# Optimization experiments

Hardware: AMD Instinct MI355X
Metric: run time of the kernel (lower is better)

## Reference

```python
import jax, jax.numpy as jnp
import numpy as np

E = 8          # num_experts
H = 1024       # hidden_size
F = 2048       # ffn_dim per expert
T = 8192       # total tokens (sorted by expert, T % E == 0)


def setup_inputs() -> dict:
    key = jax.random.key(0)
    k1, k2, k3, k4 = jax.random.split(key, 4)
    x = jax.random.normal(k1, (T, H), dtype=jnp.float32)
    # tokens are pre-sorted by expert with an equal split (dropless, balanced topo)
    expert_idx = (jnp.arange(T, dtype=jnp.int64) * E) // T
    w1 = jax.random.normal(k2, (E, F, H), dtype=jnp.float32) * 0.02
    v1 = jax.random.normal(k3, (E, F, H), dtype=jnp.float32) * 0.02
    w2 = jax.random.normal(k4, (E, F, H), dtype=jnp.float32) * 0.02
    return {"x": x, "expert_idx": expert_idx, "w1": w1, "v1": v1, "w2": w2}


def reference(x, expert_idx, w1, v1, w2):
    # Block-sparse SDD/DSD GLU with tokens grouped contiguously by expert
    # (expert_idx is sorted with equal counts), so the sparse matmuls reduce
    # to grouped batched GEMMs over the expert axis.
    tpe = x.shape[0] // w1.shape[0]          # tokens per expert
    xg = x.reshape(E, tpe, H)                # [E, tpe, H]
    # sdd(x, w1^T, topo): per-expert x @ w1_e^T  -> [E, tpe, F]
    h1 = jnp.einsum('eth,efh->etf', xg, w1)
    h2 = jnp.einsum('eth,efh->etf', xg, v1)
    # exact (erf) GELU to match torch.nn.functional.gelu default
    g = jax.nn.gelu(h1, approximate=False) * h2
    # dsd(x1, w2): per-expert g @ w2_e -> [E, tpe, H]
    out = jnp.einsum('etf,efh->eth', g, w2)
    return out.reshape(x.shape[0], H)
```

## Files before the change

kernel.cpp:

```cpp
#include <hip/hip_runtime.h>
#include <hip/hip_bf16.h>
#include <cstdint>
#include <cstddef>

#define NE 8
#define NH 1024
#define NF 2048
#define NT 8192
#define TPE (NT / NE)
#define NKT (NH / 64)
#define NKT2 (NF / 64)

typedef uint16_t u16;
typedef uint32_t u32;
typedef __attribute__((ext_vector_type(8))) __bf16 bf16x8;
typedef __attribute__((ext_vector_type(4))) float f32x4;

__device__ __forceinline__ u16 f2bf_rn(float f) {
  u32 u = __float_as_uint(f);
  u32 r = (u + 0x7fffu + ((u >> 16) & 1u)) >> 16;
  return (u16)r;
}

__global__ void cvt_f32_bf16(const float* __restrict__ in, u16* __restrict__ out, int n) {
  int i = (blockIdx.x * blockDim.x + threadIdx.x) * 4;
  if (i < n) {
    float4 v = *reinterpret_cast<const float4*>(in + i);
    ushort4 o;
    o.x = f2bf_rn(v.x);
    o.y = f2bf_rn(v.y);
    o.z = f2bf_rn(v.z);
    o.w = f2bf_rn(v.w);
    *reinterpret_cast<ushort4*>(out + i) = o;
  }
}

__global__ void pack_b(const float* __restrict__ w1, const float* __restrict__ v1,
                       u16* __restrict__ bc) {
  int j = blockIdx.x;
  int e = j >> 12;
  int r = j & 4095;
  int p = r >> 5;
  int q = (r >> 4) & 1;
  int c = r & 15;
  const float* src = (q ? v1 : w1) + ((size_t)e * NF + p * 16 + c) * NH;
  u16* dst = bc + (size_t)j * NH;
  int i = threadIdx.x * 4;
  float4 v = *reinterpret_cast<const float4*>(src + i);
  ushort4 o;
  o.x = f2bf_rn(v.x);
  o.y = f2bf_rn(v.y);
  o.z = f2bf_rn(v.z);
  o.w = f2bf_rn(v.w);
  *reinterpret_cast<ushort4*>(dst + i) = o;
}

__global__ void transpose_w2(const float* __restrict__ w2, u16* __restrict__ w2t) {
  __shared__ float tile[32][33];
  const int e = blockIdx.z;
  const int h0 = blockIdx.x * 32;
  const int f0 = blockIdx.y * 32;
  const int tx = threadIdx.x, ty = threadIdx.y;
  const float* src = w2 + ((size_t)e * NF + f0) * NH + h0;
#pragma unroll
  for (int i = 0; i < 4; i++) {
    int r = ty + i * 8;
    tile[r][tx] = src[(size_t)r * NH + tx];
  }
  __syncthreads();
  u16* dst = w2t + ((size_t)e * NH + h0) * NF + f0;
#pragma unroll
  for (int i = 0; i < 4; i++) {
    int r = ty + i * 8;
    dst[(size_t)r * NF + tx] = f2bf_rn(tile[tx][r]);
  }
}

__device__ __forceinline__ void async_lds16(const u16* g, const u16* lds) {
  __builtin_amdgcn_global_load_lds(
      (const __attribute__((address_space(1))) u32*)g,
      (__attribute__((address_space(3))) u32*)lds, 16, 0, 0);
}

__device__ __forceinline__ float one_plus_erf(float s) {
  float z = fabsf(s);
  float t = __builtin_amdgcn_rcpf(fmaf(0.3275911f, z, 1.0f));
  float p = t * fmaf(t, fmaf(t, fmaf(t, fmaf(t, 1.061405429f, -1.453152027f),
                                     1.421413741f), -0.284496736f), 0.254829592f);
  float pe = p * __expf(-z * z);
  return (s >= 0.0f) ? (2.0f - pe) : pe;
}

#define MFMA16(ACC, A, B)                                                      \
  _Pragma("unroll") for (int m = 0; m < 4; m++)                                \
    _Pragma("unroll") for (int n = 0; n < 2; n++) {                            \
      ACC[m][n] = __builtin_amdgcn_mfma_f32_16x16x32_bf16(A[m][0], B[n][0],    \
                                                          ACC[m][n], 0, 0, 0); \
      ACC[m][n] = __builtin_amdgcn_mfma_f32_16x16x32_bf16(A[m][1], B[n][1],    \
                                                          ACC[m][n], 0, 0, 0); \
    }

#define LD(OFF) (*reinterpret_cast<const bf16x8*>(Lb + (OFF)))

#define STAGE(GP, DST)                         \
  {                                            \
    async_lds16((GP) + g0, Lb + (DST) + s0);   \
    async_lds16((GP) + g1, Lb + (DST) + s1);   \
  }

__launch_bounds__(512, 2)
__global__ void glu_gemm8(const u16* __restrict__ xb, const u16* __restrict__ bc,
                          u16* __restrict__ gb) {
  __shared__ __align__(16) u16 L[2 * 2 * 2 * 8192];
  u16* Lb = &L[0];

  const int wg = blockIdx.x;
  const int sw = (wg & 7) * 64 + (wg >> 3);
  const int e = sw >> 6;
  const int by = (sw >> 4) & 3;
  const int bx = sw & 15;
  const int m0 = e * TPE + by * 256;
  const int n0 = bx * 256;

  const int tid = threadIdx.x;
  const int lane = tid & 63;
  const int wid = tid >> 6;
  const int qr = wid >> 2;
  const int qc = wid & 3;
  const int fr = lane & 15;
  const int kq = (lane >> 4) * 8;
  const int msk = (fr & 7) << 3;

  int aK0 = (qr * 64 + fr) * 64 + (kq ^ msk);
  int aK1 = (qr * 64 + fr) * 64 + ((32 + kq) ^ msk);
  int bK0 = 16384 + (qc * 32 + fr) * 64 + (kq ^ msk);
  int bK1 = 16384 + (qc * 32 + fr) * 64 + ((32 + kq) ^ msk);

  const int s0 = tid * 8;
  const int s1 = (512 + tid) * 8;
  const int r0 = s0 >> 6, r1 = s1 >> 6;
  const int g0 = r0 * NH + ((s0 & 63) ^ ((r0 & 7) << 3));
  const int g1 = r1 * NH + ((s1 & 63) ^ ((r1 & 7) << 3));

  const u16* Abase = xb + (size_t)m0 * NH;
  const u16* Bbase = bc + ((size_t)e * (2 * NF) + n0) * NH;

  f32x4 acc[2][2][4][2] = {};

  STAGE(Abase, 0);
  STAGE(Bbase, 16384);
  STAGE(Bbase + (size_t)128 * NH, 24576);
  STAGE(Abase + (size_t)128 * NH, 8192);
  STAGE(Abase + 64, 32768);
  STAGE(Bbase + (size_t)128 * NH + 64, 32768 + 24576);
  asm volatile("s_waitcnt vmcnt(4)" ::: "memory");
  __builtin_amdgcn_s_barrier();

  int bfo = 0;
#pragma unroll 1
  for (int t = 0; t < NKT; t++) {
    const int nbo = bfo ^ 32768;
    bf16x8 a_[4][2], b0_[2][2], b1_[2][2];

#pragma unroll
    for (int m = 0; m < 4; m++) {
      a_[m][0] = LD(aK0 + m * 1024);
      a_[m][1] = LD(aK1 + m * 1024);
    }
#pragma unroll
    for (int n = 0; n < 2; n++) {
      b0_[n][0] = LD(bK0 + n * 1024);
      b0_[n][1] = LD(bK1 + n * 1024);
    }
    if (t + 1 < NKT) STAGE(Abase + (size_t)128 * NH + (t + 1) * 64, nbo + 8192);
    __builtin_amdgcn_s_barrier();
    __builtin_amdgcn_s_setprio(1);
    MFMA16(acc[0][0], a_, b0_);
    __builtin_amdgcn_s_setprio(0);
    __builtin_amdgcn_s_barrier();

#pragma unroll
    for (int n = 0; n < 2; n++) {
      b1_[n][0] = LD(bK0 + 8192 + n * 1024);
      b1_[n][1] = LD(bK1 + 8192 + n * 1024);
    }
    if (t + 1 < NKT) STAGE(Bbase + (t + 1) * 64, nbo + 16384);
    __builtin_amdgcn_s_barrier();
    __builtin_amdgcn_s_setprio(1);
    MFMA16(acc[0][1], a_, b1_);
    __builtin_amdgcn_s_setprio(0);
    __builtin_amdgcn_s_barrier();

#pragma unroll
    for (int m = 0; m < 4; m++) {
      a_[m][0] = LD(aK0 + 8192 + m * 1024);
      a_[m][1] = LD(aK1 + 8192 + m * 1024);
    }
    if (t + 2 < NKT) STAGE(Abase + (t + 2) * 64, bfo);
    __builtin_amdgcn_s_barrier();
    __builtin_amdgcn_s_setprio(1);
    MFMA16(acc[1][1], a_, b1_);
    __builtin_amdgcn_s_setprio(0);
    __builtin_amdgcn_s_barrier();

    if (t + 2 < NKT) STAGE(Bbase + (size_t)128 * NH + (t + 2) * 64, bfo + 24576);
    __builtin_amdgcn_s_barrier();
    __builtin_amdgcn_s_setprio(1);
    MFMA16(acc[1][0], a_, b0_);
    __builtin_amdgcn_s_setprio(0);
    if (t + 2 < NKT)      asm volatile("s_waitcnt vmcnt(4)" ::: "memory");
    else if (t + 1 < NKT) asm volatile("s_waitcnt vmcnt(0)" ::: "memory");
    __builtin_amdgcn_s_barrier();
    aK0 ^= 32768; aK1 ^= 32768; bK0 ^= 32768; bK1 ^= 32768;
    bfo = nbo;
  }

  const int rq = (lane >> 4) * 4;
#pragma unroll
  for (int QR = 0; QR < 2; QR++)
#pragma unroll
    for (int QC = 0; QC < 2; QC++)
#pragma unroll
      for (int m = 0; m < 4; m++) {
        int row = m0 + QR * 128 + qr * 64 + m * 16 + rq;
        int f = ((n0 + QC * 128 + qc * 32) >> 1) + fr;
#pragma unroll
        for (int r = 0; r < 4; r++) {
          float h1 = acc[QR][QC][m][0][r];
          float h2 = acc[QR][QC][m][1][r];
          float g = 0.5f * h1 * one_plus_erf(h1 * 0.70710678118654752f) * h2;
          gb[(size_t)(row + r) * NF + f] = f2bf_rn(g);
        }
      }
}

__launch_bounds__(512, 2)
__global__ void down_gemm8(const u16* __restrict__ gb, const u16* __restrict__ w2tb,
                           float* __restrict__ out) {
  __shared__ __align__(16) u16 L[2 * 4 * 8192];
  u16* Lb = &L[0];

  const int wg = blockIdx.x;
  const int sw = (wg & 7) * 32 + (wg >> 3);
  const int e = sw >> 5;
  const int loc = sw & 31;
  const int bm = loc >> 2;
  const int bn = loc & 3;
  const int m0 = e * TPE + bm * 128;
  const int n0 = bn * 256;

  const int tid = threadIdx.x;
  const int lane = tid & 63;
  const int wid = tid >> 6;
  const int qr = wid >> 2;
  const int qc = wid & 3;
  const int fr = lane & 15;
  const int kq = (lane >> 4) * 8;
  const int msk = (fr & 7) << 3;

  int aK0 = (qr * 64 + fr) * 64 + (kq ^ msk);
  int aK1 = (qr * 64 + fr) * 64 + ((32 + kq) ^ msk);
  int bK0 = 8192 + (qc * 32 + fr) * 64 + (kq ^ msk);
  int bK1 = 8192 + (qc * 32 + fr) * 64 + ((32 + kq) ^ msk);

  const int s0 = tid * 8;
  const int s1 = (512 + tid) * 8;
  const int r0 = s0 >> 6, r1 = s1 >> 6;
  const int g0 = r0 * NF + ((s0 & 63) ^ ((r0 & 7) << 3));
  const int g1 = r1 * NF + ((s1 & 63) ^ ((r1 & 7) << 3));

  const u16* Ab = gb + (size_t)m0 * NF;
  const u16* Bb = w2tb + ((size_t)e * NH + n0) * NF;

  f32x4 acc[2][4][2] = {};

  STAGE(Ab, 0);
  STAGE(Bb, 8192);
  STAGE(Bb + (size_t)128 * NF, 16384);
  asm volatile("s_waitcnt vmcnt(2)" ::: "memory");
  __builtin_amdgcn_s_barrier();

  int bfo = 0;
#pragma unroll 1
  for (int t = 0; t < NKT2; t++) {
    const int nbo = bfo ^ 32768;
    bf16x8 a_[4][2], b_[2][2];

#pragma unroll
    for (int m = 0; m < 4; m++) {
      a_[m][0] = LD(aK0 + m * 1024);
      a_[m][1] = LD(aK1 + m * 1024);
    }
#pragma unroll
    for (int n = 0; n < 2; n++) {
      b_[n][0] = LD(bK0 + n * 1024);
      b_[n][1] = LD(bK1 + n * 1024);
    }
    if (t + 1 < NKT2) {
      STAGE(Ab + (t + 1) * 64, nbo);
      STAGE(Bb + (t + 1) * 64, nbo + 8192);
    }
    __builtin_amdgcn_s_barrier();
    __builtin_amdgcn_s_setprio(1);
    MFMA16(acc[0], a_, b_);
    __builtin_amdgcn_s_setprio(0);
    if (t + 1 < NKT2) asm volatile("s_waitcnt vmcnt(4)" ::: "memory");
    else              asm volatile("s_waitcnt vmcnt(0)" ::: "memory");
    __builtin_amdgcn_s_barrier();

#pragma unroll
    for (int n = 0; n < 2; n++) {
      b_[n][0] = LD(bK0 + 8192 + n * 1024);
      b_[n][1] = LD(bK1 + 8192 + n * 1024);
    }
    if (t + 1 < NKT2) STAGE(Bb + (size_t)128 * NF + (t + 1) * 64, nbo + 16384);
    __builtin_amdgcn_s_barrier();
    __builtin_amdgcn_s_setprio(1);
    MFMA16(acc[1], a_, b_);
    __builtin_amdgcn_s_setprio(0);
    if (t + 1 < NKT2) asm volatile("s_waitcnt vmcnt(2)" ::: "memory");
    __builtin_amdgcn_s_barrier();
    aK0 ^= 32768; aK1 ^= 32768; bK0 ^= 32768; bK1 ^= 32768;
    bfo = nbo;
  }

  const int rq = (lane >> 4) * 4;
#pragma unroll
  for (int QC = 0; QC < 2; QC++)
#pragma unroll
    for (int m = 0; m < 4; m++) {
      int row = m0 + qr * 64 + m * 16 + rq;
#pragma unroll
      for (int n = 0; n < 2; n++) {
        int col = n0 + QC * 128 + qc * 32 + n * 16 + fr;
#pragma unroll
        for (int r = 0; r < 4; r++)
          out[(size_t)(row + r) * NH + col] = acc[QC][m][n][r];
      }
    }
}

extern "C" void kernel_launch(void* const* d_in, const int* in_sizes, int n_in,
                              void* d_out, int out_size, void* d_ws, size_t ws_size,
                              hipStream_t stream) {
  const float* x = (const float*)d_in[0];
  const float* w1 = (const float*)d_in[2];
  const float* v1 = (const float*)d_in[3];
  const float* w2 = (const float*)d_in[4];
  float* out = (float*)d_out;

  char* ws = (char*)d_ws;
  u16* xb   = (u16*)(ws);
  u16* bc   = (u16*)(ws + (size_t)16 * 1024 * 1024);
  u16* w2tb = (u16*)(ws + (size_t)80 * 1024 * 1024);
  u16* gb   = (u16*)(ws + (size_t)112 * 1024 * 1024);

  const int nx = NT * NH;

  cvt_f32_bf16<<<nx / 4 / 256, 256, 0, stream>>>(x, xb, nx);
  pack_b<<<NE * 2 * NF, 256, 0, stream>>>(w1, v1, bc);
  transpose_w2<<<dim3(NH / 32, NF / 32, NE), dim3(32, 8, 1), 0, stream>>>(w2, w2tb);

  glu_gemm8<<<512, 512, 0, stream>>>(xb, bc, gb);
  down_gemm8<<<256, 512, 0, stream>>>(gb, w2tb, out);
}
```

Before: 175.2 us.

## Fuse prep kernels and make GLU GEMM persistent over two N tiles

Merges the three fp32-to-bf16 conversion/packing/transpose kernels into one launch with a block-index dispatch, removing two kernel launches. The GLU GEMM now runs 256 workgroups that each compute two 256-wide N tiles in sequence. The second tile's prologue loads are issued before the first tile's GELU epilogue and stores, so that global traffic overlaps the epilogue. This costs half the grid parallelism (256 blocks, one per CU) and adds register pressure from keeping the epilogue live while loads are in flight.

```diff
diff --git a/kernel.cpp b/kernel.cpp
--- a/kernel.cpp
+++ b/kernel.cpp
@@ -22,57 +22,57 @@
   return (u16)r;
 }
 
-__global__ void cvt_f32_bf16(const float* __restrict__ in, u16* __restrict__ out, int n) {
-  int i = (blockIdx.x * blockDim.x + threadIdx.x) * 4;
-  if (i < n) {
-    float4 v = *reinterpret_cast<const float4*>(in + i);
+#define PACK_NB 32768
+#define CVT_NB 8192
+#define TR_NB 16384
+
+__global__ void prep(const float* __restrict__ x, const float* __restrict__ w1,
+                     const float* __restrict__ v1, const float* __restrict__ w2,
+                     u16* __restrict__ xb, u16* __restrict__ bc, u16* __restrict__ w2t) {
+  __shared__ float tile[32][33];
+  const int bid = blockIdx.x;
+  const int tid = threadIdx.x;
+
+  if (bid < PACK_NB) {
+    int j = bid;
+    int e = j >> 12;
+    int r = j & 4095;
+    int p = r >> 5;
+    int q = (r >> 4) & 1;
+    int c = r & 15;
+    const float* src = (q ? v1 : w1) + ((size_t)e * NF + p * 16 + c) * NH;
+    u16* dst = bc + (size_t)j * NH;
+    int i = tid * 4;
+    float4 v = *reinterpret_cast<const float4*>(src + i);
     ushort4 o;
-    o.x = f2bf_rn(v.x);
-    o.y = f2bf_rn(v.y);
-    o.z = f2bf_rn(v.z);
-    o.w = f2bf_rn(v.w);
-    *reinterpret_cast<ushort4*>(out + i) = o;
-  }
-}
-
-__global__ void pack_b(const float* __restrict__ w1, const float* __restrict__ v1,
-                       u16* __restrict__ bc) {
-  int j = blockIdx.x;
-  int e = j >> 12;
-  int r = j & 4095;
-  int p = r >> 5;
-  int q = (r >> 4) & 1;
-  int c = r & 15;
-  const float* src = (q ? v1 : w1) + ((size_t)e * NF + p * 16 + c) * NH;
-  u16* dst = bc + (size_t)j * NH;
-  int i = threadIdx.x * 4;
-  float4 v = *reinterpret_cast<const float4*>(src + i);
-  ushort4 o;
-  o.x = f2bf_rn(v.x);
-  o.y = f2bf_rn(v.y);
-  o.z = f2bf_rn(v.z);
-  o.w = f2bf_rn(v.w);
-  *reinterpret_cast<ushort4*>(dst + i) = o;
-}
-
-__global__ void transpose_w2(const float* __restrict__ w2, u16* __restrict__ w2t) {
-  __shared__ float tile[32][33];
-  const int e = blockIdx.z;
-  const int h0 = blockIdx.x * 32;
-  const int f0 = blockIdx.y * 32;
-  const int tx = threadIdx.x, ty = threadIdx.y;
-  const float* src = w2 + ((size_t)e * NF + f0) * NH + h0;
-#pragma unroll
-  for (int i = 0; i < 4; i++) {
-    int r = ty + i * 8;
-    tile[r][tx] = src[(size_t)r * NH + tx];
-  }
-  __syncthreads();
-  u16* dst = w2t + ((size_t)e * NH + h0) * NF + f0;
-#pragma unroll
-  for (int i = 0; i < 4; i++) {
-    int r = ty + i * 8;
-    dst[(size_t)r * NF + tx] = f2bf_rn(tile[tx][r]);
+    o.x = f2bf_rn(v.x); o.y = f2bf_rn(v.y); o.z = f2bf_rn(v.z); o.w = f2bf_rn(v.w);
+    *reinterpret_cast<ushort4*>(dst + i) = o;
+  } else if (bid < PACK_NB + CVT_NB) {
+    int i = ((bid - PACK_NB) * 256 + tid) * 4;
+    float4 v = *reinterpret_cast<const float4*>(x + i);
+    ushort4 o;
+    o.x = f2bf_rn(v.x); o.y = f2bf_rn(v.y); o.z = f2bf_rn(v.z); o.w = f2bf_rn(v.w);
+    *reinterpret_cast<ushort4*>(xb + i) = o;
+  } else {
+    int tau = bid - (PACK_NB + CVT_NB);
+    int e = tau >> 11;
+    int w = tau & 2047;
+    int f0 = (w >> 5) * 32;
+    int h0 = (w & 31) * 32;
+    const int tx = tid & 31, ty = tid >> 5;
+    const float* src = w2 + ((size_t)e * NF + f0) * NH + h0;
+#pragma unroll
+    for (int i = 0; i < 4; i++) {
+      int r = ty + i * 8;
+      tile[r][tx] = src[(size_t)r * NH + tx];
+    }
+    __syncthreads();
+    u16* dst = w2t + ((size_t)e * NH + h0) * NF + f0;
+#pragma unroll
+    for (int i = 0; i < 4; i++) {
+      int r = ty + i * 8;
+      dst[(size_t)r * NF + tx] = f2bf_rn(tile[tx][r]);
+    }
   }
 }
 
@@ -108,6 +108,16 @@
     async_lds16((GP) + g1, Lb + (DST) + s1);   \
   }
 
+#define STAGE_PRO(BB)                                   \
+  {                                                     \
+    STAGE(Abase, 0);                                    \
+    STAGE((BB), 16384);                                 \
+    STAGE((BB) + (size_t)128 * NH, 24576);              \
+    STAGE(Abase + (size_t)128 * NH, 8192);              \
+    STAGE(Abase + 64, 32768);                           \
+    STAGE((BB) + (size_t)128 * NH + 64, 32768 + 24576); \
+  }
+
 __launch_bounds__(512, 2)
 __global__ void glu_gemm8(const u16* __restrict__ xb, const u16* __restrict__ bc,
                           u16* __restrict__ gb) {
@@ -115,12 +125,11 @@
   u16* Lb = &L[0];
 
   const int wg = blockIdx.x;
-  const int sw = (wg & 7) * 64 + (wg >> 3);
-  const int e = sw >> 6;
-  const int by = (sw >> 4) & 3;
-  const int bx = sw & 15;
+  const int sw = (wg & 7) * 32 + (wg >> 3);
+  const int e = sw >> 5;
+  const int by = (sw >> 3) & 3;
+  const int bxp = sw & 7;
   const int m0 = e * TPE + by * 256;
-  const int n0 = bx * 256;
 
   const int tid = threadIdx.x;
   const int lane = tid & 63;
@@ -131,10 +140,10 @@
   const int kq = (lane >> 4) * 8;
   const int msk = (fr & 7) << 3;
 
-  int aK0 = (qr * 64 + fr) * 64 + (kq ^ msk);
-  int aK1 = (qr * 64 + fr) * 64 + ((32 + kq) ^ msk);
-  int bK0 = 16384 + (qc * 32 + fr) * 64 + (kq ^ msk);
-  int bK1 = 16384 + (qc * 32 + fr) * 64 + ((32 + kq) ^ msk);
+  const int aB0 = (qr * 64 + fr) * 64 + (kq ^ msk);
+  const int aB1 = (qr * 64 + fr) * 64 + ((32 + kq) ^ msk);
+  const int bB0 = 16384 + (qc * 32 + fr) * 64 + (kq ^ msk);
+  const int bB1 = 16384 + (qc * 32 + fr) * 64 + ((32 + kq) ^ msk);
 
   const int s0 = tid * 8;
   const int s1 = (512 + tid) * 8;
@@ -143,95 +152,108 @@
   const int g1 = r1 * NH + ((s1 & 63) ^ ((r1 & 7) << 3));
 
   const u16* Abase = xb + (size_t)m0 * NH;
-  const u16* Bbase = bc + ((size_t)e * (2 * NF) + n0) * NH;
-
-  f32x4 acc[2][2][4][2] = {};
-
-  STAGE(Abase, 0);
-  STAGE(Bbase, 16384);
-  STAGE(Bbase + (size_t)128 * NH, 24576);
-  STAGE(Abase + (size_t)128 * NH, 8192);
-  STAGE(Abase + 64, 32768);
-  STAGE(Bbase + (size_t)128 * NH + 64, 32768 + 24576);
-  asm volatile("s_waitcnt vmcnt(4)" ::: "memory");
-  __builtin_amdgcn_s_barrier();
-
-  int bfo = 0;
+  const int rq = (lane >> 4) * 4;
+
 #pragma unroll 1
-  for (int t = 0; t < NKT; t++) {
-    const int nbo = bfo ^ 32768;
-    bf16x8 a_[4][2], b0_[2][2], b1_[2][2];
-
-#pragma unroll
-    for (int m = 0; m < 4; m++) {
-      a_[m][0] = LD(aK0 + m * 1024);
-      a_[m][1] = LD(aK1 + m * 1024);
-    }
-#pragma unroll
-    for (int n = 0; n < 2; n++) {
-      b0_[n][0] = LD(bK0 + n * 1024);
-      b0_[n][1] = LD(bK1 + n * 1024);
-    }
-    if (t + 1 < NKT) STAGE(Abase + (size_t)128 * NH + (t + 1) * 64, nbo + 8192);
-    __builtin_amdgcn_s_barrier();
-    __builtin_amdgcn_s_setprio(1);
-    MFMA16(acc[0][0], a_, b0_);
-    __builtin_amdgcn_s_setprio(0);
-    __builtin_amdgcn_s_barrier();
-
-#pragma unroll
-    for (int n = 0; n < 2; n++) {
-      b1_[n][0] = LD(bK0 + 8192 + n * 1024);
-      b1_[n][1] = LD(bK1 + 8192 + n * 1024);
-    }
-    if (t + 1 < NKT) STAGE(Bbase + (t + 1) * 64, nbo + 16384);
-    __builtin_amdgcn_s_barrier();
-    __builtin_amdgcn_s_setprio(1);
-    MFMA16(acc[0][1], a_, b1_);
-    __builtin_amdgcn_s_setprio(0);
-    __builtin_amdgcn_s_barrier();
-
-#pragma unroll
-    for (int m = 0; m < 4; m++) {
-      a_[m][0] = LD(aK0 + 8192 + m * 1024);
-      a_[m][1] = LD(aK1 + 8192 + m * 1024);
-    }
-    if (t + 2 < NKT) STAGE(Abase + (t + 2) * 64, bfo);
-    __builtin_amdgcn_s_barrier();
-    __builtin_amdgcn_s_setprio(1);
-    MFMA16(acc[1][1], a_, b1_);
-    __builtin_amdgcn_s_setprio(0);
-    __builtin_amdgcn_s_barrier();
-
-    if (t + 2 < NKT) STAGE(Bbase + (size_t)128 * NH + (t + 2) * 64, bfo + 24576);
-    __builtin_amdgcn_s_barrier();
-    __builtin_amdgcn_s_setprio(1);
-    MFMA16(acc[1][0], a_, b0_);
-    __builtin_amdgcn_s_setprio(0);
-    if (t + 2 < NKT)      asm volatile("s_waitcnt vmcnt(4)" ::: "memory");
-    else if (t + 1 < NKT) asm volatile("s_waitcnt vmcnt(0)" ::: "memory");
-    __builtin_amdgcn_s_barrier();
-    aK0 ^= 32768; aK1 ^= 32768; bK0 ^= 32768; bK1 ^= 32768;
-    bfo = nbo;
-  }
-
-  const int rq = (lane >> 4) * 4;
-#pragma unroll
-  for (int QR = 0; QR < 2; QR++)
-#pragma unroll
-    for (int QC = 0; QC < 2; QC++)
+  for (int tt = 0; tt < 2; tt++) {
+    const int n0 = (bxp + tt * 8) * 256;
+    const u16* Bbase = bc + ((size_t)e * (2 * NF) + n0) * NH;
+
+    if (tt == 0) {
+      STAGE_PRO(Bbase);
+      asm volatile("s_waitcnt vmcnt(4)" ::: "memory");
+      __builtin_amdgcn_s_barrier();
+    }
+
+    f32x4 acc[2][2][4][2] = {};
+    int aK0 = aB0, aK1 = aB1, bK0 = bB0, bK1 = bB1;
+    int bfo = 0;
+
+#pragma unroll 1
+    for (int t = 0; t < NKT; t++) {
+      const int nbo = bfo ^ 32768;
+      bf16x8 a_[4][2], b0_[2][2], b1_[2][2];
+
 #pragma unroll
       for (int m = 0; m < 4; m++) {
-        int row = m0 + QR * 128 + qr * 64 + m * 16 + rq;
-        int f = ((n0 + QC * 128 + qc * 32) >> 1) + fr;
-#pragma unroll
-        for (int r = 0; r < 4; r++) {
-          float h1 = acc[QR][QC][m][0][r];
-          float h2 = acc[QR][QC][m][1][r];
-          float g = 0.5f * h1 * one_plus_erf(h1 * 0.70710678118654752f) * h2;
-          gb[(size_t)(row + r) * NF + f] = f2bf_rn(g);
+        a_[m][0] = LD(aK0 + m * 1024);
+        a_[m][1] = LD(aK1 + m * 1024);
+      }
+#pragma unroll
+      for (int n = 0; n < 2; n++) {
+        b0_[n][0] = LD(bK0 + n * 1024);
+        b0_[n][1] = LD(bK1 + n * 1024);
+      }
+      if (t + 1 < NKT) STAGE(Abase + (size_t)128 * NH + (t + 1) * 64, nbo + 8192);
+      __builtin_amdgcn_s_barrier();
+      __builtin_amdgcn_s_setprio(1);
+      MFMA16(acc[0][0], a_, b0_);
+      __builtin_amdgcn_s_setprio(0);
+      __builtin_amdgcn_s_barrier();
+
+#pragma unroll
+      for (int n = 0; n < 2; n++) {
+        b1_[n][0] = LD(bK0 + 8192 + n * 1024);
+        b1_[n][1] = LD(bK1 + 8192 + n * 1024);
+      }
+      if (t + 1 < NKT) STAGE(Bbase + (t + 1) * 64, nbo + 16384);
+      __builtin_amdgcn_s_barrier();
+      __builtin_amdgcn_s_setprio(1);
+      MFMA16(acc[0][1], a_, b1_);
+      __builtin_amdgcn_s_setprio(0);
+      __builtin_amdgcn_s_barrier();
+
+#pragma unroll
+      for (int m = 0; m < 4; m++) {
+        a_[m][0] = LD(aK0 + 8192 + m * 1024);
+        a_[m][1] = LD(aK1 + 8192 + m * 1024);
+      }
+      if (t + 2 < NKT) STAGE(Abase + (t + 2) * 64, bfo);
+      __builtin_amdgcn_s_barrier();
+      __builtin_amdgcn_s_setprio(1);
+      MFMA16(acc[1][1], a_, b1_);
+      __builtin_amdgcn_s_setprio(0);
+      __builtin_amdgcn_s_barrier();
+
+      if (t + 2 < NKT) STAGE(Bbase + (size_t)128 * NH + (t + 2) * 64, bfo + 24576);
+      __builtin_amdgcn_s_barrier();
+      __builtin_amdgcn_s_setprio(1);
+      MFMA16(acc[1][0], a_, b0_);
+      __builtin_amdgcn_s_setprio(0);
+      if (t + 2 < NKT)      asm volatile("s_waitcnt vmcnt(4)" ::: "memory");
+      else if (t + 1 < NKT) asm volatile("s_waitcnt vmcnt(0)" ::: "memory");
+      __builtin_amdgcn_s_barrier();
+      aK0 ^= 32768; aK1 ^= 32768; bK0 ^= 32768; bK1 ^= 32768;
+      bfo = nbo;
+    }
+
+    if (tt == 0) {
+      const u16* Bb2 = bc + ((size_t)e * (2 * NF) + (bxp + 8) * 256) * NH;
+      STAGE_PRO(Bb2);
+    }
+
+#pragma unroll
+    for (int QR = 0; QR < 2; QR++)
+#pragma unroll
+      for (int QC = 0; QC < 2; QC++)
+#pragma unroll
+        for (int m = 0; m < 4; m++) {
+          int row = m0 + QR * 128 + qr * 64 + m * 16 + rq;
+          int f = ((n0 + QC * 128 + qc * 32) >> 1) + fr;
+#pragma unroll
+          for (int r = 0; r < 4; r++) {
+            float h1 = acc[QR][QC][m][0][r];
+            float h2 = acc[QR][QC][m][1][r];
+            float g = 0.5f * h1 * one_plus_erf(h1 * 0.70710678118654752f) * h2;
+            gb[(size_t)(row + r) * NF + f] = f2bf_rn(g);
+          }
         }
-      }
+
+    if (tt == 0) {
+      asm volatile("s_waitcnt vmcnt(0)" ::: "memory");
+      __builtin_amdgcn_s_barrier();
+    }
+  }
 }
 
 __launch_bounds__(512, 2)
@@ -355,12 +377,7 @@
   u16* w2tb = (u16*)(ws + (size_t)80 * 1024 * 1024);
   u16* gb   = (u16*)(ws + (size_t)112 * 1024 * 1024);
 
-  const int nx = NT * NH;
-
-  cvt_f32_bf16<<<nx / 4 / 256, 256, 0, stream>>>(x, xb, nx);
-  pack_b<<<NE * 2 * NF, 256, 0, stream>>>(w1, v1, bc);
-  transpose_w2<<<dim3(NH / 32, NF / 32, NE), dim3(32, 8, 1), 0, stream>>>(w2, w2tb);
-
-  glu_gemm8<<<512, 512, 0, stream>>>(xb, bc, gb);
+  prep<<<PACK_NB + CVT_NB + TR_NB, 256, 0, stream>>>(x, w1, v1, w2, xb, bc, w2tb);
+  glu_gemm8<<<256, 512, 0, stream>>>(xb, bc, gb);
   down_gemm8<<<256, 512, 0, stream>>>(gb, w2tb, out);
 }
```

New measurement: 187.4 us. 7.0% more time.
